# Performance work log

Hardware: AMD Instinct MI355X
Metric: run time of the kernel (lower is better)

The kernel has to match this reference:

```python
import jax, jax.numpy as jnp
import numpy as np

D_MODEL = 1024
N_INPUT = 4096
N_PROCESS = 2048
D_ROUTING = 256
TEMPERATURE = 0.5
LN_EPS = 1e-5


def _gelu(x):
    return jax.nn.gelu(x, approximate=False)  # torch F.gelu default (erf)


def setup_inputs() -> dict:
    key = jax.random.key(0)
    ks = jax.random.split(key, 10)
    B, S = 8, 2048
    x = jax.random.normal(ks[0], (B, S, D_MODEL), dtype=jnp.float32)
    # GlobalRouter query_net: Linear(d_model, 2*d_routing) -> GELU -> LayerNorm -> Linear(2*d_routing, d_routing)
    W1 = jax.random.normal(ks[1], (2 * D_ROUTING, D_MODEL), dtype=jnp.float32) * (2.0 / (D_MODEL + 2 * D_ROUTING)) ** 0.5 * 1.414
    b1 = jnp.zeros((2 * D_ROUTING,), dtype=jnp.float32)
    ln_g = jnp.ones((2 * D_ROUTING,), dtype=jnp.float32)
    ln_b = jnp.zeros((2 * D_ROUTING,), dtype=jnp.float32)
    W2 = jax.random.normal(ks[2], (D_ROUTING, 2 * D_ROUTING), dtype=jnp.float32) * (2.0 / (3 * D_ROUTING)) ** 0.5 * 1.414
    b2 = jnp.zeros((D_ROUTING,), dtype=jnp.float32)
    neuron_keys = jax.random.normal(ks[3], (N_INPUT, D_ROUTING), dtype=jnp.float32) / D_ROUTING ** 0.5 * 1.414
    input_patterns = jax.random.normal(ks[4], (N_INPUT, D_MODEL), dtype=jnp.float32) / D_MODEL ** 0.5 * 1.414
    process_weights = jax.random.normal(ks[5], (N_PROCESS, N_INPUT), dtype=jnp.float32) / N_INPUT ** 0.5 * 1.414
    process_outputs = jax.random.normal(ks[6], (N_PROCESS, D_MODEL), dtype=jnp.float32) / D_MODEL ** 0.5 * 1.414
    return {
        'x': x, 'k_input': 2048, 'k_process': 1024,
        'W1': W1, 'b1': b1, 'ln_g': ln_g, 'ln_b': ln_b, 'W2': W2, 'b2': b2,
        'neuron_keys': neuron_keys, 'input_patterns': input_patterns,
        'process_weights': process_weights, 'process_outputs': process_outputs,
    }


def _forward(x, k_input, k_process, W1, b1, ln_g, ln_b, W2, b2,
             neuron_keys, input_patterns, process_weights, process_outputs):
    B, S, d_model = x.shape
    # ---- GlobalRouter ----
    gctx = jnp.max(x, axis=1)                                  # [B, d_model]
    h = _gelu(gctx @ W1.T + b1)                                # [B, 2*d_routing]
    mu = jnp.mean(h, axis=-1, keepdims=True)
    var = jnp.mean((h - mu) ** 2, axis=-1, keepdims=True)
    h = (h - mu) * jax.lax.rsqrt(var + LN_EPS) * ln_g + ln_b
    query = h @ W2.T + b2                                      # [B, d_routing]
    logits = (query @ neuron_keys.T) / D_ROUTING ** 0.5        # [B, n_input]
    probs = jax.nn.softmax(logits / TEMPERATURE, axis=-1)
    _, input_idx = jax.lax.top_k(logits, k_input)              # [B, k_input]
    one_hot = jnp.zeros_like(probs).at[jnp.arange(B)[:, None], input_idx].set(1.0)
    routing_weights = jax.lax.stop_gradient(one_hot - probs) + probs  # STE
    # ---- input neuron stage ----
    input_acts = _gelu(jnp.einsum('bsd,nd->bsn', x, input_patterns))   # [B,S,n_input]
    weighted = input_acts * routing_weights[:, None, :]
    sel_in = jnp.take_along_axis(weighted, input_idx[:, None, :], axis=2)  # [B,S,k_input]
    # gather process weight columns per batch: [B, n_process, k_input]
    W_sel = jnp.transpose(process_weights[:, input_idx], (1, 0, 2))
    process_acts = _gelu(jnp.einsum('bsk,bpk->bsp', sel_in, W_sel))    # [B,S,n_process]
    # ---- process neuron stage ----
    process_scores = jnp.mean(process_acts, axis=1)                    # [B,n_process]
    _, process_idx = jax.lax.top_k(process_scores, k_process)          # [B,k_process]
    sel_proc = jnp.take_along_axis(process_acts, process_idx[:, None, :], axis=2)  # [B,S,k_process]
    out_sel = process_outputs[process_idx]                             # [B,k_process,d_model]
    return jnp.einsum('bsp,bpd->bsd', sel_proc, out_sel)


def reference(x, k_input, k_process, W1, b1, ln_g, ln_b, W2, b2,
              neuron_keys, input_patterns, process_weights, process_outputs):
    return _forward(x, k_input, k_process, W1, b1, ln_g, ln_b, W2, b2,
                    neuron_keys, input_patterns, process_weights, process_outputs)
```

## Files before the change

kernel.cpp:

```cpp
#include <hip/hip_runtime.h>
#include <stdint.h>

#define B_  8
#define S_  2048
#define DM  1024
#define NI  4096
#define NP  2048
#define DR  256
#define H2  512
#define KI  2048
#define KP  1024
#define LDW 40

typedef __attribute__((ext_vector_type(8))) short bf16x8;
typedef __attribute__((ext_vector_type(4))) float f32x4;
typedef unsigned short ushort;
typedef unsigned int uint;

__device__ __forceinline__ float gelu_erf(float v){
    return 0.5f * v * (1.0f + erff(v * 0.7071067811865476f));
}
__device__ __forceinline__ ushort f2b(float f){
    union { float f; uint u; } a; a.f = f;
    uint r = a.u + 0x7fffu + ((a.u >> 16) & 1u);
    return (ushort)(r >> 16);
}
__device__ __forceinline__ float b2f(ushort u){
    union { uint u; float f; } a; a.u = ((uint)u) << 16; return a.f;
}
__device__ __forceinline__ void cvt8(const float* p, uint4& H, uint4& L){
    uint h[4], l[4];
    #pragma unroll
    for(int i = 0; i < 4; i++){
        ushort h0 = f2b(p[2*i]);   float f0 = b2f(h0); ushort l0 = f2b(p[2*i]   - f0);
        ushort h1 = f2b(p[2*i+1]); float f1 = b2f(h1); ushort l1 = f2b(p[2*i+1] - f1);
        h[i] = (uint)h0 | ((uint)h1 << 16);
        l[i] = (uint)l0 | ((uint)l1 << 16);
    }
    H = uint4{h[0],h[1],h[2],h[3]};
    L = uint4{l[0],l[1],l[2],l[3]};
}

__global__ __launch_bounds__(256) void k_gpart(const float* __restrict__ x,
                                               float* __restrict__ gpart){
    int b = blockIdx.x >> 4, ch = blockIdx.x & 15;
    const float4* xb = (const float4*)(x + ((size_t)b*S_ + (size_t)ch*128) * DM);
    int t = threadIdx.x;
    float4 m = xb[t];
    for(int r = 1; r < 128; r++){
        float4 v = xb[(size_t)r*(DM/4) + t];
        m.x = fmaxf(m.x, v.x); m.y = fmaxf(m.y, v.y);
        m.z = fmaxf(m.z, v.z); m.w = fmaxf(m.w, v.w);
    }
    ((float4*)(gpart + (size_t)(b*16 + ch)*DM))[t] = m;
}

__global__ __launch_bounds__(256) void k_h(const float* __restrict__ gpart,
                                           const float* __restrict__ W1,
                                           const float* __restrict__ b1,
                                           float* __restrict__ h){
    __shared__ float g[DM];
    int b = blockIdx.x >> 3, ig = blockIdx.x & 7;
    int t = threadIdx.x;
    for(int d = t; d < DM; d += 256){
        float m = gpart[(size_t)(b*16)*DM + d];
        for(int c = 1; c < 16; c++) m = fmaxf(m, gpart[(size_t)(b*16 + c)*DM + d]);
        g[d] = m;
    }
    __syncthreads();
    int i  = ig*64 + (t >> 2);
    int dq = (t & 3) * 256;
    const float* wr = W1 + (size_t)i*DM + dq;
    const float* gg = g + dq;
    float s = 0.f;
    for(int d = 0; d < 256; d++) s = fmaf(gg[d], wr[d], s);
    s += __shfl_xor(s, 1);
    s += __shfl_xor(s, 2);
    if((t & 3) == 0) h[b*H2 + i] = gelu_erf(s + b1[i]);
}

__global__ __launch_bounds__(256) void k_query(const float* __restrict__ h,
                                               const float* __restrict__ lng,
                                               const float* __restrict__ lnb,
                                               const float* __restrict__ W2,
                                               const float* __restrict__ b2,
                                               float* __restrict__ query){
    __shared__ float hn[H2];
    __shared__ float red[4];
    int b = blockIdx.x >> 2, qg = blockIdx.x & 3;
    int t = threadIdx.x;
    float v0 = h[b*H2 + t], v1 = h[b*H2 + 256 + t];
    float s = v0 + v1;
    for(int o = 32; o > 0; o >>= 1) s += __shfl_down(s, o);
    if((t & 63) == 0) red[t >> 6] = s;
    __syncthreads();
    float mean = (red[0] + red[1] + red[2] + red[3]) * (1.f/H2);
    __syncthreads();
    float d0 = v0 - mean, d1 = v1 - mean;
    float sq = d0*d0 + d1*d1;
    for(int o = 32; o > 0; o >>= 1) sq += __shfl_down(sq, o);
    if((t & 63) == 0) red[t >> 6] = sq;
    __syncthreads();
    float var  = (red[0] + red[1] + red[2] + red[3]) * (1.f/H2);
    float rstd = rsqrtf(var + 1e-5f);
    hn[t]       = d0*rstd*lng[t]       + lnb[t];
    hn[256 + t] = d1*rstd*lng[256 + t] + lnb[256 + t];
    __syncthreads();
    int q  = qg*64 + (t >> 2);
    int iq = (t & 3) * 128;
    const float* wr = W2 + (size_t)q*H2 + iq;
    float acc = 0.f;
    for(int i2 = 0; i2 < 128; i2++) acc = fmaf(hn[iq + i2], wr[i2], acc);
    acc += __shfl_xor(acc, 1);
    acc += __shfl_xor(acc, 2);
    if((t & 3) == 0) query[b*DR + q] = acc + b2[q];
}

__global__ __launch_bounds__(256) void k_logits(const float* __restrict__ query,
                                                const float* __restrict__ nk,
                                                float* __restrict__ logits){
    __shared__ float q[DR];
    int b = blockIdx.x >> 4, ng = blockIdx.x & 15;
    int t = threadIdx.x;
    if(t < DR) q[t] = query[b*DR + t];
    __syncthreads();
    int n = ng*256 + t;
    const float* kr = nk + (size_t)n*DR;
    float s = 0.f;
    for(int i = 0; i < DR; i++) s = fmaf(q[i], kr[i], s);
    logits[b*NI + n] = s * 0.0625f;
}

template<int N_, int KSEL>
__global__ __launch_bounds__(256) void k_topk(const float* __restrict__ vals,
                                              int* __restrict__ idxout){
    __shared__ unsigned u[N_];
    __shared__ int redc[4];
    __shared__ int sc[256];
    int t = threadIdx.x;
    size_t vbase = (size_t)blockIdx.x * N_;
    size_t obase = (size_t)blockIdx.x * KSEL;
    for(int i = t; i < N_; i += 256){
        unsigned bits = __float_as_uint(vals[vbase + i]);
        u[i] = (bits & 0x80000000u) ? ~bits : (bits | 0x80000000u);
    }
    __syncthreads();
    unsigned lo = 0u, hi = 0xFFFFFFFFu;
    while(lo < hi){
        unsigned mid = lo + (unsigned)((((unsigned long long)(hi - lo)) + 1ull) >> 1);
        int c = 0;
        for(int i = t; i < N_; i += 256) c += (u[i] >= mid) ? 1 : 0;
        for(int o = 32; o > 0; o >>= 1) c += __shfl_down(c, o);
        if((t & 63) == 0) redc[t >> 6] = c;
        __syncthreads();
        int tot = redc[0] + redc[1] + redc[2] + redc[3];
        if(tot >= KSEL) lo = mid; else hi = mid - 1;
        __syncthreads();
    }
    unsigned T = lo;
    const int PER = N_ / 256;
    int base = t * PER;
    int lgt = 0, leq = 0;
    for(int j = 0; j < PER; j++){
        unsigned v = u[base + j];
        lgt += (v > T) ? 1 : 0; leq += (v == T) ? 1 : 0;
    }
    sc[t] = (lgt << 16) | leq;
    __syncthreads();
    for(int o = 1; o < 256; o <<= 1){
        int add = (t >= o) ? sc[t - o] : 0;
        __syncthreads();
        sc[t] += add;
        __syncthreads();
    }
    int need = KSEL - (sc[255] >> 16);
    int ex = (t == 0) ? 0 : sc[t - 1];
    int pos = (ex >> 16) + ((ex & 0xffff) < need ? (ex & 0xffff) : need);
    int eq = ex & 0xffff;
    for(int j = 0; j < PER; j++){
        unsigned v = u[base + j];
        if(v > T){ idxout[obase + pos++] = base + j; }
        else if(v == T){ if(eq < need){ idxout[obase + pos++] = base + j; } eq++; }
    }
}

__global__ __launch_bounds__(256) void k_gemm1(const float* __restrict__ x,
                                               const float* __restrict__ patt,
                                               const int* __restrict__ iidx,
                                               ushort* __restrict__ selh,
                                               ushort* __restrict__ sell, int b0){
    __shared__ __align__(16) ushort Ah[128*LDW], Al[128*LDW], Bh[128*LDW], Bl[128*LDW];
    __shared__ int rowmap[128];
    int t = threadIdx.x;
    int g = blockIdx.x >> 8, rest = blockIdx.x & 255;
    int b = b0 + g;
    int mb = rest >> 4, nb = rest & 15;
    int m0 = mb*128, n0 = nb*128;
    ushort* selh_g = selh + (size_t)g*S_*KI;
    ushort* sell_g = sell + (size_t)g*S_*KI;
    if(t < 128) rowmap[t] = iidx[(size_t)b*KI + n0 + t];
    __syncthreads();
    int r = t & 127, half = t >> 7;
    const float* ag = x    + (size_t)b*S_*DM + (size_t)(m0 + r)*DM + half*16;
    const float* bg = patt + (size_t)rowmap[r]*DM + half*16;
    float4 fa[4], fb[4];
    #pragma unroll
    for(int i = 0; i < 4; i++){ fa[i] = *(const float4*)(ag + i*4); fb[i] = *(const float4*)(bg + i*4); }
    int w = t >> 6, lane = t & 63;
    int mbase = (w >> 1)*64, nbase = (w & 1)*64;
    int lm = lane & 15, q = lane >> 4;
    f32x4 acc[4][4];
    #pragma unroll
    for(int i = 0; i < 4; i++)
      #pragma unroll
      for(int j = 0; j < 4; j++) acc[i][j] = f32x4{0.f,0.f,0.f,0.f};
    for(int k0 = 0; k0 < DM; k0 += 32){
        uint4 AH0, AL0, AH1, AL1, BH0, BL0, BH1, BL1;
        cvt8((const float*)&fa[0], AH0, AL0); cvt8((const float*)&fa[2], AH1, AL1);
        cvt8((const float*)&fb[0], BH0, BL0); cvt8((const float*)&fb[2], BH1, BL1);
        __syncthreads();
        *(uint4*)(Ah + r*LDW + half*16)     = AH0;
        *(uint4*)(Ah + r*LDW + half*16 + 8) = AH1;
        *(uint4*)(Al + r*LDW + half*16)     = AL0;
        *(uint4*)(Al + r*LDW + half*16 + 8) = AL1;
        *(uint4*)(Bh + r*LDW + half*16)     = BH0;
        *(uint4*)(Bh + r*LDW + half*16 + 8) = BH1;
        *(uint4*)(Bl + r*LDW + half*16)     = BL0;
        *(uint4*)(Bl + r*LDW + half*16 + 8) = BL1;
        __syncthreads();
        if(k0 + 32 < DM){
            ag += 32; bg += 32;
            #pragma unroll
            for(int i = 0; i < 4; i++){ fa[i] = *(const float4*)(ag + i*4); fb[i] = *(const float4*)(bg + i*4); }
        }
        bf16x8 ahf[4], alf[4];
        #pragma unroll
        for(int mt = 0; mt < 4; mt++){
            ahf[mt] = *(const bf16x8*)(Ah + (mbase + mt*16 + lm)*LDW + q*8);
            alf[mt] = *(const bf16x8*)(Al + (mbase + mt*16 + lm)*LDW + q*8);
        }
        #pragma unroll
        for(int nt = 0; nt < 4; nt++){
            bf16x8 bhf = *(const bf16x8*)(Bh + (nbase + nt*16 + lm)*LDW + q*8);
            bf16x8 blf = *(const bf16x8*)(Bl + (nbase + nt*16 + lm)*LDW + q*8);
            #pragma unroll
            for(int mt = 0; mt < 4; mt++){
                acc[mt][nt] = __builtin_amdgcn_mfma_f32_16x16x32_bf16(ahf[mt], bhf, acc[mt][nt], 0, 0, 0);
                acc[mt][nt] = __builtin_amdgcn_mfma_f32_16x16x32_bf16(ahf[mt], blf, acc[mt][nt], 0, 0, 0);
                acc[mt][nt] = __builtin_amdgcn_mfma_f32_16x16x32_bf16(alf[mt], bhf, acc[mt][nt], 0, 0, 0);
            }
        }
    }
    #pragma unroll
    for(int mt = 0; mt < 4; mt++)
      #pragma unroll
      for(int nt = 0; nt < 4; nt++){
        int col = n0 + nbase + nt*16 + lm;
        #pragma unroll
        for(int i = 0; i < 4; i++){
            int row = m0 + mbase + mt*16 + q*4 + i;
            float gv = gelu_erf(acc[mt][nt][i]);
            ushort hbits = f2b(gv);
            selh_g[(size_t)row*KI + col] = hbits;
            sell_g[(size_t)row*KI + col] = f2b(gv - b2f(hbits));
        }
      }
}

__global__ __launch_bounds__(256) void k_gather_wsel(const float* __restrict__ pw,
                                                     const int* __restrict__ iidx,
                                                     ushort* __restrict__ wh,
                                                     ushort* __restrict__ wl,
                                                     float* __restrict__ scores, int b0){
    __shared__ int kidx[KI];
    int g = blockIdx.x >> 8, pc = blockIdx.x & 255;
    int b = b0 + g;
    ushort* wh_g = wh + (size_t)g*NP*KI;
    ushort* wl_g = wl + (size_t)g*NP*KI;
    int t = threadIdx.x;
    for(int i = t; i < KI; i += 256) kidx[i] = iidx[(size_t)b*KI + i];
    if(t < 8) scores[(size_t)b*NP + pc*8 + t] = 0.f;
    __syncthreads();
    for(int r2 = 0; r2 < 8; r2++){
        int p = pc*8 + r2;
        const float* row = pw + (size_t)p*NI;
        for(int j = t; j < KI; j += 256){
            float v = row[kidx[j]];
            ushort hb = f2b(v);
            wh_g[(size_t)p*KI + j] = hb;
            wl_g[(size_t)p*KI + j] = f2b(v - b2f(hb));
        }
    }
}

__global__ __launch_bounds__(256) void k_gemm2(const ushort* __restrict__ selh,
                                               const ushort* __restrict__ sell,
                                               const ushort* __restrict__ wh,
                                               const ushort* __restrict__ wl,
                                               ushort* __restrict__ acts,
                                               float* __restrict__ scores, int b0){
    __shared__ __align__(16) ushort Ah[128*LDW], Al[128*LDW], Bh[128*LDW], Bl[128*LDW];
    __shared__ float colsum[128];
    int t = threadIdx.x;
    int g = blockIdx.x >> 8, rest = blockIdx.x & 255;
    int b = b0 + g;
    int mb = rest >> 4, nb = rest & 15;
    int m0 = mb*128, n0 = nb*128;
    const ushort* selh_g = selh + (size_t)g*S_*KI;
    const ushort* sell_g = sell + (size_t)g*S_*KI;
    const ushort* wh_g   = wh   + (size_t)g*NP*KI;
    const ushort* wl_g   = wl   + (size_t)g*NP*KI;
    ushort* acts_g = acts + (size_t)g*S_*NP;
    int r = t & 127, half = t >> 7;
    const ushort* ahg = selh_g + (size_t)(m0 + r)*KI + half*16;
    const ushort* alg = sell_g + (size_t)(m0 + r)*KI + half*16;
    const ushort* bhg = wh_g   + (size_t)(n0 + r)*KI + half*16;
    const ushort* blg = wl_g   + (size_t)(n0 + r)*KI + half*16;
    uint4 AH0, AH1, AL0, AL1, BH0, BH1, BL0, BL1;
    AH0 = *(const uint4*)(ahg); AH1 = *(const uint4*)(ahg + 8);
    AL0 = *(const uint4*)(alg); AL1 = *(const uint4*)(alg + 8);
    BH0 = *(const uint4*)(bhg); BH1 = *(const uint4*)(bhg + 8);
    BL0 = *(const uint4*)(blg); BL1 = *(const uint4*)(blg + 8);
    int w = t >> 6, lane = t & 63;
    int mbase = (w >> 1)*64, nbase = (w & 1)*64;
    int lm = lane & 15, q = lane >> 4;
    f32x4 acc[4][4];
    #pragma unroll
    for(int i = 0; i < 4; i++)
      #pragma unroll
      for(int j = 0; j < 4; j++) acc[i][j] = f32x4{0.f,0.f,0.f,0.f};
    for(int k0 = 0; k0 < KI; k0 += 32){
        __syncthreads();
        *(uint4*)(Ah + r*LDW + half*16)     = AH0;
        *(uint4*)(Ah + r*LDW + half*16 + 8) = AH1;
        *(uint4*)(Al + r*LDW + half*16)     = AL0;
        *(uint4*)(Al + r*LDW + half*16 + 8) = AL1;
        *(uint4*)(Bh + r*LDW + half*16)     = BH0;
        *(uint4*)(Bh + r*LDW + half*16 + 8) = BH1;
        *(uint4*)(Bl + r*LDW + half*16)     = BL0;
        *(uint4*)(Bl + r*LDW + half*16 + 8) = BL1;
        __syncthreads();
        if(k0 + 32 < KI){
            ahg += 32; alg += 32; bhg += 32; blg += 32;
            AH0 = *(const uint4*)(ahg); AH1 = *(const uint4*)(ahg + 8);
            AL0 = *(const uint4*)(alg); AL1 = *(const uint4*)(alg + 8);
            BH0 = *(const uint4*)(bhg); BH1 = *(const uint4*)(bhg + 8);
            BL0 = *(const uint4*)(blg); BL1 = *(const uint4*)(blg + 8);
        }
        bf16x8 ahf[4], alf[4];
        #pragma unroll
        for(int mt = 0; mt < 4; mt++){
            ahf[mt] = *(const bf16x8*)(Ah + (mbase + mt*16 + lm)*LDW + q*8);
            alf[mt] = *(const bf16x8*)(Al + (mbase + mt*16 + lm)*LDW + q*8);
        }
        #pragma unroll
        for(int nt = 0; nt < 4; nt++){
            bf16x8 bhf = *(const bf16x8*)(Bh + (nbase + nt*16 + lm)*LDW + q*8);
            bf16x8 blf = *(const bf16x8*)(Bl + (nbase + nt*16 + lm)*LDW + q*8);
            #pragma unroll
            for(int mt = 0; mt < 4; mt++){
                acc[mt][nt] = __builtin_amdgcn_mfma_f32_16x16x32_bf16(ahf[mt], bhf, acc[mt][nt], 0, 0, 0);
                acc[mt][nt] = __builtin_amdgcn_mfma_f32_16x16x32_bf16(ahf[mt], blf, acc[mt][nt], 0, 0, 0);
                acc[mt][nt] = __builtin_amdgcn_mfma_f32_16x16x32_bf16(alf[mt], bhf, acc[mt][nt], 0, 0, 0);
            }
        }
    }
    if(t < 128) colsum[t] = 0.f;
    __syncthreads();
    #pragma unroll
    for(int mt = 0; mt < 4; mt++)
      #pragma unroll
      for(int nt = 0; nt < 4; nt++){
        int cb = nbase + nt*16 + lm;
        float s4 = 0.f;
        #pragma unroll
        for(int i = 0; i < 4; i++){
            int row = m0 + mbase + mt*16 + q*4 + i;
            float gv = gelu_erf(acc[mt][nt][i]);
            s4 += gv;
            acts_g[(size_t)row*NP + n0 + cb] = f2b(gv);
        }
        atomicAdd(&colsum[cb], s4);
      }
    __syncthreads();
    if(t < 128) atomicAdd(&scores[(size_t)b*NP + n0 + t], colsum[t]);
}

__global__ __launch_bounds__(256) void k_gather_selacts(const ushort* __restrict__ acts,
                                                        const int* __restrict__ pidx,
                                                        ushort* __restrict__ selacts, int b0){
    __shared__ int pix[KP];
    int g = blockIdx.x >> 6, sc_ = blockIdx.x & 63;
    int b = b0 + g;
    const ushort* acts_g = acts + (size_t)g*S_*NP;
    ushort* selacts_g = selacts + (size_t)g*S_*KP;
    int t = threadIdx.x;
    for(int i = t; i < KP; i += 256) pix[i] = pidx[(size_t)b*KP + i];
    __syncthreads();
    const ushort* Ab = acts_g    + ((size_t)sc_*32)*NP;
    ushort*       Ob = selacts_g + ((size_t)sc_*32)*KP;
    for(int r2 = 0; r2 < 32; r2++){
        for(int j = t; j < KP; j += 256)
            Ob[(size_t)r2*KP + j] = Ab[(size_t)r2*NP + pix[j]];
    }
}

__global__ __launch_bounds__(256) void k_gemm3(const ushort* __restrict__ selacts,
                                               const float* __restrict__ pout,
                                               const int* __restrict__ pidx,
                                               float* __restrict__ out, int b0){
    __shared__ __align__(16) ushort As[128*LDW], Bs[128*LDW];
    __shared__ int pix[KP];
    int t = threadIdx.x;
    int g = blockIdx.x >> 7, rest = blockIdx.x & 127;
    int b = b0 + g;
    int mb = rest >> 3, nb = rest & 7;
    int m0 = mb*128, n0 = nb*128;
    const ushort* selacts_g = selacts + (size_t)g*S_*KP;
    for(int i = t; i < KP; i += 256) pix[i] = pidx[(size_t)b*KP + i];
    __syncthreads();
    int r = t & 127, half = t >> 7;
    const ushort* ag = selacts_g + (size_t)(m0 + r)*KP + half*16;
    int kk = t >> 3, nc = (t & 7)*16;
    uint4 A0 = *(const uint4*)(ag), A1 = *(const uint4*)(ag + 8);
    float4 fb[4];
    {
        const float* bg = pout + (size_t)pix[kk]*DM + n0 + nc;
        #pragma unroll
        for(int i = 0; i < 4; i++) fb[i] = *(const float4*)(bg + i*4);
    }
    int w = t >> 6, lane = t & 63;
    int mbase = (w >> 1)*64, nbase = (w & 1)*64;
    int lm = lane & 15, q = lane >> 4;
    f32x4 acc[4][4];
    #pragma unroll
    for(int i = 0; i < 4; i++)
      #pragma unroll
      for(int j = 0; j < 4; j++) acc[i][j] = f32x4{0.f,0.f,0.f,0.f};
    for(int k0 = 0; k0 < KP; k0 += 32){
        __syncthreads();
        *(uint4*)(As + r*LDW + half*16)     = A0;
        *(uint4*)(As + r*LDW + half*16 + 8) = A1;
        {
            const float* pf = (const float*)fb;
            #pragma unroll
            for(int c = 0; c < 16; c++) Bs[(nc + c)*LDW + kk] = f2b(pf[c]);
        }
        __syncthreads();
        if(k0 + 32 < KP){
            ag += 32;
            A0 = *(const uint4*)(ag); A1 = *(const uint4*)(ag + 8);
            const float* bg = pout + (size_t)pix[k0 + 32 + kk]*DM + n0 + nc;
            #pragma unroll
            for(int i = 0; i < 4; i++) fb[i] = *(const float4*)(bg + i*4);
        }
        bf16x8 af[4];
        #pragma unroll
        for(int mt = 0; mt < 4; mt++)
            af[mt] = *(const bf16x8*)(As + (mbase + mt*16 + lm)*LDW + q*8);
        #pragma unroll
        for(int nt = 0; nt < 4; nt++){
            bf16x8 bf = *(const bf16x8*)(Bs + (nbase + nt*16 + lm)*LDW + q*8);
            #pragma unroll
            for(int mt = 0; mt < 4; mt++)
                acc[mt][nt] = __builtin_amdgcn_mfma_f32_16x16x32_bf16(af[mt], bf, acc[mt][nt], 0, 0, 0);
        }
    }
    float* Cb = out + (size_t)b*S_*DM;
    #pragma unroll
    for(int mt = 0; mt < 4; mt++)
      #pragma unroll
      for(int nt = 0; nt < 4; nt++){
        int col = n0 + nbase + nt*16 + lm;
        #pragma unroll
        for(int i = 0; i < 4; i++){
            int row = m0 + mbase + mt*16 + q*4 + i;
            Cb[(size_t)row*DM + col] = acc[mt][nt][i];
        }
      }
}

extern "C" void kernel_launch(void* const* d_in, const int* in_sizes, int n_in,
                              void* d_out, int out_size, void* d_ws, size_t ws_size,
                              hipStream_t stream){
    const float* x    = (const float*)d_in[0];
    const float* W1   = (const float*)d_in[3];
    const float* b1   = (const float*)d_in[4];
    const float* lng  = (const float*)d_in[5];
    const float* lnb  = (const float*)d_in[6];
    const float* W2   = (const float*)d_in[7];
    const float* b2   = (const float*)d_in[8];
    const float* nk   = (const float*)d_in[9];
    const float* patt = (const float*)d_in[10];
    const float* pw   = (const float*)d_in[11];
    const float* pout = (const float*)d_in[12];
    float* out = (float*)d_out;

    const size_t fixed =
        ((size_t)B_*16*DM*4 + 255 & ~(size_t)255) + ((size_t)B_*H2*4 + 255 & ~(size_t)255) +
        ((size_t)B_*DR*4 + 255 & ~(size_t)255)    + ((size_t)B_*NI*4 + 255 & ~(size_t)255) +
        ((size_t)B_*KI*4 + 255 & ~(size_t)255)    + ((size_t)B_*NP*4 + 255 & ~(size_t)255) +
        ((size_t)B_*KP*4 + 255 & ~(size_t)255);
    const size_t perb = (size_t)S_*KI*2*2 + (size_t)NP*KI*2*2 + (size_t)S_*NP*2 + (size_t)S_*KP*2 + 6*256;
    int G = 4;
    while(G > 1 && fixed + (size_t)G*perb > ws_size) G >>= 1;
    if(fixed + (size_t)G*perb > ws_size) return;

    char* wsp = (char*)d_ws;
    size_t off = 0;
    auto alloc = [&](size_t bytes) -> void* {
        void* p = wsp + off;
        off += (bytes + 255) & ~(size_t)255;
        return p;
    };
    float*  gpart   = (float*) alloc((size_t)B_*16*DM*4);
    float*  h       = (float*) alloc((size_t)B_*H2*4);
    float*  query   = (float*) alloc((size_t)B_*DR*4);
    float*  logits  = (float*) alloc((size_t)B_*NI*4);
    int*    iidx    = (int*)   alloc((size_t)B_*KI*4);
    float*  scores  = (float*) alloc((size_t)B_*NP*4);
    int*    pidx    = (int*)   alloc((size_t)B_*KP*4);
    ushort* selh    = (ushort*)alloc((size_t)G*S_*KI*2);
    ushort* sell    = (ushort*)alloc((size_t)G*S_*KI*2);
    ushort* wselh   = (ushort*)alloc((size_t)G*NP*KI*2);
    ushort* wsell   = (ushort*)alloc((size_t)G*NP*KI*2);
    ushort* acts    = (ushort*)alloc((size_t)G*S_*NP*2);
    ushort* selacts = (ushort*)alloc((size_t)G*S_*KP*2);

    dim3 blk(256);
    k_gpart <<<128, blk, 0, stream>>>(x, gpart);
    k_h     <<<64,  blk, 0, stream>>>(gpart, W1, b1, h);
    k_query <<<32,  blk, 0, stream>>>(h, lng, lnb, W2, b2, query);
    k_logits<<<128, blk, 0, stream>>>(query, nk, logits);
    k_topk<NI, KI><<<B_, blk, 0, stream>>>(logits, iidx);
    for(int b0 = 0; b0 < B_; b0 += G){
        k_gemm1        <<<G*256, blk, 0, stream>>>(x, patt, iidx, selh, sell, b0);
        k_gather_wsel  <<<G*256, blk, 0, stream>>>(pw, iidx, wselh, wsell, scores, b0);
        k_gemm2        <<<G*256, blk, 0, stream>>>(selh, sell, wselh, wsell, acts, scores, b0);
        k_topk<NP, KP> <<<G,     blk, 0, stream>>>(scores + (size_t)b0*NP, pidx + (size_t)b0*KP);
        k_gather_selacts<<<G*64, blk, 0, stream>>>(acts, pidx, selacts, b0);
        k_gemm3        <<<G*128, blk, 0, stream>>>(selacts, pout, pidx, out, b0);
    }
}
```

Before: 1.509 ms.

## Pre-split inputs to bf16 and double-buffer GEMM tiles via direct global-to-LDS loads

Adds a conversion kernel that splits x and input_patterns into bf16 hi/lo arrays once up front. Before this, gemm1 redid the fp32-to-bf16 split inside every tile, and each x tile was converted again by all 16 column blocks. gemm1 and gemm2 now stage tiles with global_load_lds straight into double-buffered LDS, so the next k-slice loads while the MFMAs run. Raised wave priority and explicit waitcnt/barrier replace the register round-trip and the two syncthreads per step. The trade-offs are extra workspace and memory traffic for the pre-split copies, and an unpadded LDS row stride that may cause bank conflicts.

```diff
diff --git a/kernel.cpp b/kernel.cpp
--- a/kernel.cpp
+++ b/kernel.cpp
@@ -39,6 +39,22 @@
     }
     H = uint4{h[0],h[1],h[2],h[3]};
     L = uint4{l[0],l[1],l[2],l[3]};
+}
+__device__ __forceinline__ void gload_lds16(const void* g, void* l){
+    __builtin_amdgcn_global_load_lds((const __attribute__((address_space(1))) void*)g,
+                                     (__attribute__((address_space(3))) void*)l, 16, 0, 0);
+}
+
+__global__ __launch_bounds__(256) void k_cvt(const float* __restrict__ src,
+                                             ushort* __restrict__ hi,
+                                             ushort* __restrict__ lo){
+    size_t idx = (size_t)blockIdx.x*256 + threadIdx.x;
+    float f[8];
+    *(float4*)(f)     = ((const float4*)src)[idx*2];
+    *(float4*)(f + 4) = ((const float4*)src)[idx*2 + 1];
+    uint4 H, L; cvt8(f, H, L);
+    ((uint4*)hi)[idx] = H;
+    ((uint4*)lo)[idx] = L;
 }
 
 __global__ __launch_bounds__(256) void k_gpart(const float* __restrict__ x,
@@ -184,12 +200,14 @@
     }
 }
 
-__global__ __launch_bounds__(256) void k_gemm1(const float* __restrict__ x,
-                                               const float* __restrict__ patt,
+__global__ __launch_bounds__(256) void k_gemm1(const ushort* __restrict__ xh,
+                                               const ushort* __restrict__ xl,
+                                               const ushort* __restrict__ ph,
+                                               const ushort* __restrict__ pl,
                                                const int* __restrict__ iidx,
                                                ushort* __restrict__ selh,
                                                ushort* __restrict__ sell, int b0){
-    __shared__ __align__(16) ushort Ah[128*LDW], Al[128*LDW], Bh[128*LDW], Bl[128*LDW];
+    __shared__ __align__(16) ushort Ah[2][128*32], Al[2][128*32], Bh[2][128*32], Bl[2][128*32];
     __shared__ int rowmap[128];
     int t = threadIdx.x;
     int g = blockIdx.x >> 8, rest = blockIdx.x & 255;
@@ -200,49 +218,57 @@
     ushort* sell_g = sell + (size_t)g*S_*KI;
     if(t < 128) rowmap[t] = iidx[(size_t)b*KI + n0 + t];
     __syncthreads();
-    int r = t & 127, half = t >> 7;
-    const float* ag = x    + (size_t)b*S_*DM + (size_t)(m0 + r)*DM + half*16;
-    const float* bg = patt + (size_t)rowmap[r]*DM + half*16;
-    float4 fa[4], fb[4];
-    #pragma unroll
-    for(int i = 0; i < 4; i++){ fa[i] = *(const float4*)(ag + i*4); fb[i] = *(const float4*)(bg + i*4); }
-    int w = t >> 6, lane = t & 63;
+    int w = t >> 6, l = t & 63;
+    int lr = l >> 2, lc = l & 3;
+    int r0 = 32*w + lr, r1 = r0 + 16;
+    const ushort* pAh0 = xh + ((size_t)b*S_ + m0 + r0)*DM + lc*8;
+    const ushort* pAh1 = xh + ((size_t)b*S_ + m0 + r1)*DM + lc*8;
+    const ushort* pAl0 = xl + ((size_t)b*S_ + m0 + r0)*DM + lc*8;
+    const ushort* pAl1 = xl + ((size_t)b*S_ + m0 + r1)*DM + lc*8;
+    const ushort* pBh0 = ph + (size_t)rowmap[r0]*DM + lc*8;
+    const ushort* pBh1 = ph + (size_t)rowmap[r1]*DM + lc*8;
+    const ushort* pBl0 = pl + (size_t)rowmap[r0]*DM + lc*8;
+    const ushort* pBl1 = pl + (size_t)rowmap[r1]*DM + lc*8;
+    int d0 = w*1024, d1 = d0 + 512;
+    #define STG1(BUF, KO) do{ \
+        gload_lds16(pAh0 + (KO), &Ah[BUF][d0]); \
+        gload_lds16(pAh1 + (KO), &Ah[BUF][d1]); \
+        gload_lds16(pAl0 + (KO), &Al[BUF][d0]); \
+        gload_lds16(pAl1 + (KO), &Al[BUF][d1]); \
+        gload_lds16(pBh0 + (KO), &Bh[BUF][d0]); \
+        gload_lds16(pBh1 + (KO), &Bh[BUF][d1]); \
+        gload_lds16(pBl0 + (KO), &Bl[BUF][d0]); \
+        gload_lds16(pBl1 + (KO), &Bl[BUF][d1]); \
+    }while(0)
+    STG1(0, 0);
+    int lm = l & 15, q = l >> 4;
     int mbase = (w >> 1)*64, nbase = (w & 1)*64;
-    int lm = lane & 15, q = lane >> 4;
     f32x4 acc[4][4];
     #pragma unroll
     for(int i = 0; i < 4; i++)
       #pragma unroll
       for(int j = 0; j < 4; j++) acc[i][j] = f32x4{0.f,0.f,0.f,0.f};
+    int cur = 0;
     for(int k0 = 0; k0 < DM; k0 += 32){
-        uint4 AH0, AL0, AH1, AL1, BH0, BL0, BH1, BL1;
-        cvt8((const float*)&fa[0], AH0, AL0); cvt8((const float*)&fa[2], AH1, AL1);
-        cvt8((const float*)&fb[0], BH0, BL0); cvt8((const float*)&fb[2], BH1, BL1);
-        __syncthreads();
-        *(uint4*)(Ah + r*LDW + half*16)     = AH0;
-        *(uint4*)(Ah + r*LDW + half*16 + 8) = AH1;
-        *(uint4*)(Al + r*LDW + half*16)     = AL0;
-        *(uint4*)(Al + r*LDW + half*16 + 8) = AL1;
-        *(uint4*)(Bh + r*LDW + half*16)     = BH0;
-        *(uint4*)(Bh + r*LDW + half*16 + 8) = BH1;
-        *(uint4*)(Bl + r*LDW + half*16)     = BL0;
-        *(uint4*)(Bl + r*LDW + half*16 + 8) = BL1;
-        __syncthreads();
         if(k0 + 32 < DM){
-            ag += 32; bg += 32;
-            #pragma unroll
-            for(int i = 0; i < 4; i++){ fa[i] = *(const float4*)(ag + i*4); fb[i] = *(const float4*)(bg + i*4); }
-        }
+            STG1(cur^1, k0 + 32);
+            asm volatile("s_waitcnt vmcnt(8)" ::: "memory");
+        }else{
+            asm volatile("s_waitcnt vmcnt(0)" ::: "memory");
+        }
+        __builtin_amdgcn_s_barrier();
+        asm volatile("" ::: "memory");
         bf16x8 ahf[4], alf[4];
         #pragma unroll
         for(int mt = 0; mt < 4; mt++){
-            ahf[mt] = *(const bf16x8*)(Ah + (mbase + mt*16 + lm)*LDW + q*8);
-            alf[mt] = *(const bf16x8*)(Al + (mbase + mt*16 + lm)*LDW + q*8);
-        }
+            ahf[mt] = *(const bf16x8*)(&Ah[cur][(mbase + mt*16 + lm)*32 + q*8]);
+            alf[mt] = *(const bf16x8*)(&Al[cur][(mbase + mt*16 + lm)*32 + q*8]);
+        }
+        __builtin_amdgcn_s_setprio(1);
         #pragma unroll
         for(int nt = 0; nt < 4; nt++){
-            bf16x8 bhf = *(const bf16x8*)(Bh + (nbase + nt*16 + lm)*LDW + q*8);
-            bf16x8 blf = *(const bf16x8*)(Bl + (nbase + nt*16 + lm)*LDW + q*8);
+            bf16x8 bhf = *(const bf16x8*)(&Bh[cur][(nbase + nt*16 + lm)*32 + q*8]);
+            bf16x8 blf = *(const bf16x8*)(&Bl[cur][(nbase + nt*16 + lm)*32 + q*8]);
             #pragma unroll
             for(int mt = 0; mt < 4; mt++){
                 acc[mt][nt] = __builtin_amdgcn_mfma_f32_16x16x32_bf16(ahf[mt], bhf, acc[mt][nt], 0, 0, 0);
@@ -250,7 +276,13 @@
                 acc[mt][nt] = __builtin_amdgcn_mfma_f32_16x16x32_bf16(alf[mt], bhf, acc[mt][nt], 0, 0, 0);
             }
         }
-    }
+        __builtin_amdgcn_s_setprio(0);
+        asm volatile("s_waitcnt lgkmcnt(0)" ::: "memory");
+        __builtin_amdgcn_s_barrier();
+        asm volatile("" ::: "memory");
+        cur ^= 1;
+    }
+    #undef STG1
     #pragma unroll
     for(int mt = 0; mt < 4; mt++)
       #pragma unroll
@@ -299,7 +331,7 @@
                                                const ushort* __restrict__ wl,
                                                ushort* __restrict__ acts,
                                                float* __restrict__ scores, int b0){
-    __shared__ __align__(16) ushort Ah[128*LDW], Al[128*LDW], Bh[128*LDW], Bl[128*LDW];
+    __shared__ __align__(16) ushort Ah[2][128*32], Al[2][128*32], Bh[2][128*32], Bl[2][128*32];
     __shared__ float colsum[128];
     int t = threadIdx.x;
     int g = blockIdx.x >> 8, rest = blockIdx.x & 255;
@@ -311,52 +343,57 @@
     const ushort* wh_g   = wh   + (size_t)g*NP*KI;
     const ushort* wl_g   = wl   + (size_t)g*NP*KI;
     ushort* acts_g = acts + (size_t)g*S_*NP;
-    int r = t & 127, half = t >> 7;
-    const ushort* ahg = selh_g + (size_t)(m0 + r)*KI + half*16;
-    const ushort* alg = sell_g + (size_t)(m0 + r)*KI + half*16;
-    const ushort* bhg = wh_g   + (size_t)(n0 + r)*KI + half*16;
-    const ushort* blg = wl_g   + (size_t)(n0 + r)*KI + half*16;
-    uint4 AH0, AH1, AL0, AL1, BH0, BH1, BL0, BL1;
-    AH0 = *(const uint4*)(ahg); AH1 = *(const uint4*)(ahg + 8);
-    AL0 = *(const uint4*)(alg); AL1 = *(const uint4*)(alg + 8);
-    BH0 = *(const uint4*)(bhg); BH1 = *(const uint4*)(bhg + 8);
-    BL0 = *(const uint4*)(blg); BL1 = *(const uint4*)(blg + 8);
-    int w = t >> 6, lane = t & 63;
+    int w = t >> 6, l = t & 63;
+    int lr = l >> 2, lc = l & 3;
+    int r0 = 32*w + lr, r1 = r0 + 16;
+    const ushort* pAh0 = selh_g + (size_t)(m0 + r0)*KI + lc*8;
+    const ushort* pAh1 = selh_g + (size_t)(m0 + r1)*KI + lc*8;
+    const ushort* pAl0 = sell_g + (size_t)(m0 + r0)*KI + lc*8;
+    const ushort* pAl1 = sell_g + (size_t)(m0 + r1)*KI + lc*8;
+    const ushort* pBh0 = wh_g + (size_t)(n0 + r0)*KI + lc*8;
+    const ushort* pBh1 = wh_g + (size_t)(n0 + r1)*KI + lc*8;
+    const ushort* pBl0 = wl_g + (size_t)(n0 + r0)*KI + lc*8;
+    const ushort* pBl1 = wl_g + (size_t)(n0 + r1)*KI + lc*8;
+    int d0 = w*1024, d1 = d0 + 512;
+    #define STG2(BUF, KO) do{ \
+        gload_lds16(pAh0 + (KO), &Ah[BUF][d0]); \
+        gload_lds16(pAh1 + (KO), &Ah[BUF][d1]); \
+        gload_lds16(pAl0 + (KO), &Al[BUF][d0]); \
+        gload_lds16(pAl1 + (KO), &Al[BUF][d1]); \
+        gload_lds16(pBh0 + (KO), &Bh[BUF][d0]); \
+        gload_lds16(pBh1 + (KO), &Bh[BUF][d1]); \
+        gload_lds16(pBl0 + (KO), &Bl[BUF][d0]); \
+        gload_lds16(pBl1 + (KO), &Bl[BUF][d1]); \
+    }while(0)
+    STG2(0, 0);
+    int lm = l & 15, q = l >> 4;
     int mbase = (w >> 1)*64, nbase = (w & 1)*64;
-    int lm = lane & 15, q = lane >> 4;
     f32x4 acc[4][4];
     #pragma unroll
     for(int i = 0; i < 4; i++)
       #pragma unroll
       for(int j = 0; j < 4; j++) acc[i][j] = f32x4{0.f,0.f,0.f,0.f};
+    int cur = 0;
     for(int k0 = 0; k0 < KI; k0 += 32){
-        __syncthreads();
-        *(uint4*)(Ah + r*LDW + half*16)     = AH0;
-        *(uint4*)(Ah + r*LDW + half*16 + 8) = AH1;
-        *(uint4*)(Al + r*LDW + half*16)     = AL0;
-        *(uint4*)(Al + r*LDW + half*16 + 8) = AL1;
-        *(uint4*)(Bh + r*LDW + half*16)     = BH0;
-        *(uint4*)(Bh + r*LDW + half*16 + 8) = BH1;
-        *(uint4*)(Bl + r*LDW + half*16)     = BL0;
-        *(uint4*)(Bl + r*LDW + half*16 + 8) = BL1;
-        __syncthreads();
         if(k0 + 32 < KI){
-            ahg += 32; alg += 32; bhg += 32; blg += 32;
-            AH0 = *(const uint4*)(ahg); AH1 = *(const uint4*)(ahg + 8);
-            AL0 = *(const uint4*)(alg); AL1 = *(const uint4*)(alg + 8);
-            BH0 = *(const uint4*)(bhg); BH1 = *(const uint4*)(bhg + 8);
-            BL0 = *(const uint4*)(blg); BL1 = *(const uint4*)(blg + 8);
-        }
+            STG2(cur^1, k0 + 32);
+            asm volatile("s_waitcnt vmcnt(8)" ::: "memory");
+        }else{
+            asm volatile("s_waitcnt vmcnt(0)" ::: "memory");
+        }
+        __builtin_amdgcn_s_barrier();
+        asm volatile("" ::: "memory");
         bf16x8 ahf[4], alf[4];
         #pragma unroll
         for(int mt = 0; mt < 4; mt++){
-            ahf[mt] = *(const bf16x8*)(Ah + (mbase + mt*16 + lm)*LDW + q*8);
-            alf[mt] = *(const bf16x8*)(Al + (mbase + mt*16 + lm)*LDW + q*8);
-        }
+            ahf[mt] = *(const bf16x8*)(&Ah[cur][(mbase + mt*16 + lm)*32 + q*8]);
+            alf[mt] = *(const bf16x8*)(&Al[cur][(mbase + mt*16 + lm)*32 + q*8]);
+        }
+        __builtin_amdgcn_s_setprio(1);
         #pragma unroll
         for(int nt = 0; nt < 4; nt++){
-            bf16x8 bhf = *(const bf16x8*)(Bh + (nbase + nt*16 + lm)*LDW + q*8);
-            bf16x8 blf = *(const bf16x8*)(Bl + (nbase + nt*16 + lm)*LDW + q*8);
+            bf16x8 bhf = *(const bf16x8*)(&Bh[cur][(nbase + nt*16 + lm)*32 + q*8]);
+            bf16x8 blf = *(const bf16x8*)(&Bl[cur][(nbase + nt*16 + lm)*32 + q*8]);
             #pragma unroll
             for(int mt = 0; mt < 4; mt++){
                 acc[mt][nt] = __builtin_amdgcn_mfma_f32_16x16x32_bf16(ahf[mt], bhf, acc[mt][nt], 0, 0, 0);
@@ -364,7 +401,13 @@
                 acc[mt][nt] = __builtin_amdgcn_mfma_f32_16x16x32_bf16(alf[mt], bhf, acc[mt][nt], 0, 0, 0);
             }
         }
-    }
+        __builtin_amdgcn_s_setprio(0);
+        asm volatile("s_waitcnt lgkmcnt(0)" ::: "memory");
+        __builtin_amdgcn_s_barrier();
+        asm volatile("" ::: "memory");
+        cur ^= 1;
+    }
+    #undef STG2
     if(t < 128) colsum[t] = 0.f;
     __syncthreads();
     #pragma unroll
@@ -496,11 +539,12 @@
     const float* pout = (const float*)d_in[12];
     float* out = (float*)d_out;
 
+    auto al256 = [](size_t v){ return (v + 255) & ~(size_t)255; };
     const size_t fixed =
-        ((size_t)B_*16*DM*4 + 255 & ~(size_t)255) + ((size_t)B_*H2*4 + 255 & ~(size_t)255) +
-        ((size_t)B_*DR*4 + 255 & ~(size_t)255)    + ((size_t)B_*NI*4 + 255 & ~(size_t)255) +
-        ((size_t)B_*KI*4 + 255 & ~(size_t)255)    + ((size_t)B_*NP*4 + 255 & ~(size_t)255) +
-        ((size_t)B_*KP*4 + 255 & ~(size_t)255);
+        al256((size_t)B_*16*DM*4) + al256((size_t)B_*H2*4) + al256((size_t)B_*DR*4) +
+        al256((size_t)B_*NI*4)    + al256((size_t)B_*KI*4) + al256((size_t)B_*NP*4) +
+        al256((size_t)B_*KP*4) +
+        2*al256((size_t)B_*S_*DM*2) + 2*al256((size_t)NI*DM*2);
     const size_t perb = (size_t)S_*KI*2*2 + (size_t)NP*KI*2*2 + (size_t)S_*NP*2 + (size_t)S_*KP*2 + 6*256;
     int G = 4;
     while(G > 1 && fixed + (size_t)G*perb > ws_size) G >>= 1;
@@ -520,6 +564,10 @@
     int*    iidx    = (int*)   alloc((size_t)B_*KI*4);
     float*  scores  = (float*) alloc((size_t)B_*NP*4);
     int*    pidx    = (int*)   alloc((size_t)B_*KP*4);
+    ushort* xh      = (ushort*)alloc((size_t)B_*S_*DM*2);
+    ushort* xl      = (ushort*)alloc((size_t)B_*S_*DM*2);
+    ushort* patth   = (ushort*)alloc((size_t)NI*DM*2);
+    ushort* pattl   = (ushort*)alloc((size_t)NI*DM*2);
     ushort* selh    = (ushort*)alloc((size_t)G*S_*KI*2);
     ushort* sell    = (ushort*)alloc((size_t)G*S_*KI*2);
     ushort* wselh   = (ushort*)alloc((size_t)G*NP*KI*2);
@@ -528,13 +576,15 @@
     ushort* selacts = (ushort*)alloc((size_t)G*S_*KP*2);
 
     dim3 blk(256);
+    k_cvt   <<<(B_*S_*DM/8)/256, blk, 0, stream>>>(x, xh, xl);
+    k_cvt   <<<(NI*DM/8)/256,    blk, 0, stream>>>(patt, patth, pattl);
     k_gpart <<<128, blk, 0, stream>>>(x, gpart);
     k_h     <<<64,  blk, 0, stream>>>(gpart, W1, b1, h);
     k_query <<<32,  blk, 0, stream>>>(h, lng, lnb, W2, b2, query);
     k_logits<<<128, blk, 0, stream>>>(query, nk, logits);
     k_topk<NI, KI><<<B_, blk, 0, stream>>>(logits, iidx);
     for(int b0 = 0; b0 < B_; b0 += G){
-        k_gemm1        <<<G*256, blk, 0, stream>>>(x, patt, iidx, selh, sell, b0);
+        k_gemm1        <<<G*256, blk, 0, stream>>>(xh, xl, patth, pattl, iidx, selh, sell, b0);
         k_gather_wsel  <<<G*256, blk, 0, stream>>>(pw, iidx, wselh, wsell, scores, b0);
         k_gemm2        <<<G*256, blk, 0, stream>>>(selh, sell, wselh, wsell, acts, scores, b0);
         k_topk<NP, KP> <<<G,     blk, 0, stream>>>(scores + (size_t)b0*NP, pidx + (size_t)b0*KP);
```

After: 1.465 ms. 2.9% less time.
